# Performance work log

Hardware: AMD Instinct MI355X
Metric: run time of the kernel (lower is better)

The kernel has to match this reference:

```python
import jax, jax.numpy as jnp
import numpy as np

B, S, D, H, DH = 8192, 64, 32, 4, 8

def setup_inputs() -> dict:
    key = jax.random.key(0)
    ks = jax.random.split(key, 10)
    lim = 1.0 / np.sqrt(D)
    def lin(k):
        kw, kb = jax.random.split(k)
        W = jax.random.uniform(kw, (D, D), jnp.float32, -lim, lim)
        b = jax.random.uniform(kb, (D,), jnp.float32, -lim, lim)
        return W, b
    Wq, bq = lin(ks[0]); Wk, bk = lin(ks[1]); Wv, bv = lin(ks[2]); Wp, bp = lin(ks[3])
    x = jax.random.normal(ks[4], (B, S, D), jnp.float32)
    always_attend_upto = jax.random.randint(ks[5], (B,), 0, 64, jnp.int64 if jax.config.jax_enable_x64 else jnp.int32)
    return {"x": x, "always_attend_upto": always_attend_upto,
            "Wq": Wq, "bq": bq, "Wk": Wk, "bk": bk, "Wv": Wv, "bv": bv, "Wp": Wp, "bp": bp}

def reference(x, always_attend_upto, Wq, bq, Wk, bk, Wv, bv, Wp, bp):
    # QKV projections (torch Linear: y = x @ W.T + b)
    def heads(W, b):
        y = x @ W.T + b                      # [B,S,D]
        return y.reshape(B, S, H, DH).transpose(0, 2, 1, 3)  # [B,H,S,DH]
    q, k, v = heads(Wq, bq), heads(Wk, bk), heads(Wv, bv)
    score = jnp.einsum('bhqd,bhkd->bhqk', q, k) / jnp.sqrt(jnp.float32(DH))
    # prefix-LM mask: allowed if causal (j<=i) OR key in prefix (j < length[b])
    i = jnp.arange(S)[:, None]
    j = jnp.arange(S)[None, :]
    causal = j <= i                                        # [S,S]
    prefix = j[None, :, :] < always_attend_upto[:, None, None]  # [B,S,S]
    allowed = (causal[None] | prefix)[:, None, :, :]       # [B,1,S,S]
    score = jnp.where(allowed, score, -jnp.inf)
    attn = jax.nn.softmax(score, axis=-1)
    out = jnp.einsum('bhqk,bhkd->bhqd', attn, v)           # [B,H,S,DH]
    out = out.transpose(0, 2, 1, 3).reshape(B, S, D)
    return out @ Wp.T + bp
```

## Files before the change

### kernel.cpp

```cpp
#include <hip/hip_runtime.h>
#include <cstdint>
#include <cstddef>

#define NB 8192

typedef __attribute__((ext_vector_type(8))) short short8;
typedef __attribute__((ext_vector_type(4))) float f32x4;

union S8U { short8 s; unsigned u[4]; uint4 v; };
union FI { float f; int i; unsigned u; };

static __device__ __forceinline__ unsigned pk2(float a, float b) {
    unsigned short ua = __builtin_bit_cast(unsigned short, (__bf16)a);
    unsigned short ub = __builtin_bit_cast(unsigned short, (__bf16)b);
    return (unsigned)ua | ((unsigned)ub << 16);
}

#define MFMA __builtin_amdgcn_mfma_f32_16x16x32_bf16
#define BPERM __builtin_amdgcn_ds_bpermute
#define LDSFENCE() asm volatile("" ::: "memory")

__global__ __launch_bounds__(128, 4) void fused_attn_mfma(
    const float* __restrict__ x,
    const int*   __restrict__ aatt,
    const float* __restrict__ Wq, const float* __restrict__ bq,
    const float* __restrict__ Wk, const float* __restrict__ bk,
    const float* __restrict__ Wv, const float* __restrict__ bv,
    const float* __restrict__ Wp, const float* __restrict__ bp,
    float* __restrict__ out)
{
    __shared__ __align__(16) short klds[64][40];
    __shared__ __align__(16) short vbt[33][72];
    __shared__ __align__(16) short psl[2][16][40];

    const int tid  = threadIdx.x;
    const int w    = tid >> 6;
    const int lane = tid & 63;
    const int q4   = lane >> 4;
    const int l15  = lane & 15;
    const int b    = blockIdx.x;

    const int aab = aatt[b];
    const unsigned bmask = (q4 == 0) ? 0xFFFFFFFFu : 0u;

    int cmpv[4];
#pragma unroll
    for (int it = 0; it < 4; ++it) cmpv[it] = max(l15 + 16*it, aab - 1) - q4*4;

    short8 xa[4];
    const float* xb = x + (size_t)b * 64 * 32;
#pragma unroll
    for (int nt = 0; nt < 4; ++nt) {
        const float* p = xb + (nt*16 + l15)*32 + q4*8;
        float4 u0 = *(const float4*)p;
        float4 u1 = *(const float4*)(p + 4);
        S8U t;
        t.u[0] = pk2(u0.x, u0.y); t.u[1] = pk2(u0.z, u0.w);
        t.u[2] = pk2(u1.x, u1.y); t.u[3] = pk2(u1.z, u1.w);
        xa[nt] = t.s;
    }

    auto wrow = [&](const float* W, int row) -> short8 {
        const float* p = W + row*32 + q4*8;
        float4 u0 = *(const float4*)p;
        float4 u1 = *(const float4*)(p + 4);
        S8U t;
        t.u[0] = pk2(u0.x, u0.y); t.u[1] = pk2(u0.z, u0.w);
        t.u[2] = pk2(u1.x, u1.y); t.u[3] = pk2(u1.z, u1.w);
        return t.s;
    };

    const float escale = 0.35355339059327373f * 1.4426950408889634f;

    unsigned qpk01[4], qpk23[4];
    {
        short8 wa = wrow(Wq, 16*w + l15);
        float4 b4 = *(const float4*)(bq + 16*w + q4*4);
#pragma unroll
        for (int nt = 0; nt < 4; ++nt) {
            f32x4 acc = {0.f,0.f,0.f,0.f};
            acc = MFMA(wa, xa[nt], acc, 0,0,0);
            qpk01[nt] = pk2((acc[0]+b4.x)*escale, (acc[1]+b4.y)*escale);
            qpk23[nt] = pk2((acc[2]+b4.z)*escale, (acc[3]+b4.w)*escale);
        }
    }
    {
        short8 wa = wrow(Wk, 16*w + l15);
        float4 b4 = *(const float4*)(bk + 16*w + q4*4);
#pragma unroll
        for (int nt = 0; nt < 4; ++nt) {
            f32x4 acc = {0.f,0.f,0.f,0.f};
            acc = MFMA(wa, xa[nt], acc, 0,0,0);
            uint2 w2;
            w2.x = pk2(acc[0]+b4.x, acc[1]+b4.y);
            w2.y = pk2(acc[2]+b4.z, acc[3]+b4.w);
            *(uint2*)&klds[nt*16 + l15][16*w + q4*4] = w2;
        }
    }
    {
        short8 wv = wrow(Wv, 16*w + l15);
        const float bvv = bv[16*w + l15];
#pragma unroll
        for (int mt = 0; mt < 4; ++mt) {
            f32x4 acc = {0.f,0.f,0.f,0.f};
            acc = MFMA(xa[mt], wv, acc, 0,0,0);
            uint2 w2;
            w2.x = pk2(acc[0]+bvv, acc[1]+bvv);
            w2.y = pk2(acc[2]+bvv, acc[3]+bvv);
            *(uint2*)&vbt[16*w + l15][mt*16 + q4*4] = w2;
        }
    }
    if (q4 == 0) {
        uint2 ones; ones.x = 0x3F803F80u; ones.y = 0x3F803F80u;
        *(uint2*)&vbt[32][l15*4] = ones;
    }
    LDSFENCE();

    unsigned opk01s[2][4], opk23s[2][4];

#pragma unroll
    for (int hl = 0; hl < 2; ++hl) {
        const int idxA = (32*hl + l15) * 4;
        const int idxB = idxA + 64;

        short8 sqb[4];
#pragma unroll
        for (int it = 0; it < 4; ++it) {
            S8U t;
            t.u[0] = (unsigned)BPERM(idxA, (int)qpk01[it]) & bmask;
            t.u[1] = (unsigned)BPERM(idxA, (int)qpk23[it]) & bmask;
            t.u[2] = (unsigned)BPERM(idxB, (int)qpk01[it]) & bmask;
            t.u[3] = (unsigned)BPERM(idxB, (int)qpk23[it]) & bmask;
            sqb[it] = t.s;
        }

        const int avrow = (l15 < 8) ? (16*w + 8*hl + l15) : 32;
        const short* avbase = &vbt[avrow][0];

        f32x4 oacch[4];
#pragma unroll
        for (int it = 0; it < 4; ++it) oacch[it] = (f32x4){0.f,0.f,0.f,0.f};

#pragma unroll
        for (int jb = 0; jb < 2; ++jb) {
            short8 ska[2];
#pragma unroll
            for (int jt = 0; jt < 2; ++jt) {
                S8U t; t.v = *(const uint4*)&klds[jb*32 + jt*16 + l15][16*w + 8*hl];
                ska[jt] = t.s;
            }
            S8U av; av.v = *(const uint4*)&avbase[jb*32 + q4*8];

#pragma unroll
            for (int it = 0; it < 4; ++it) {
#pragma unroll
                for (int jt = 0; jt < 2; ++jt) {
                    f32x4 sacc = {0.f,0.f,0.f,0.f};
                    sacc = MFMA(ska[jt], sqb[it], sacc, 0,0,0);
                    float e[4];
#pragma unroll
                    for (int r = 0; r < 4; ++r) {
                        float ee = __builtin_amdgcn_exp2f(sacc[r]);
                        e[r] = (jb*32 + jt*16 + r <= cmpv[it]) ? ee : 0.0f;
                    }
                    uint2 pw; pw.x = pk2(e[0], e[1]); pw.y = pk2(e[2], e[3]);
                    *(uint2*)&psl[w][l15][jt*16 + q4*4] = pw;
                }
                LDSFENCE();
                S8U pb; pb.v = *(const uint4*)&psl[w][l15][q4*8];
                oacch[it] = MFMA(av.s, pb.s, oacch[it], 0,0,0);
                LDSFENCE();
            }
        }

#pragma unroll
        for (int it = 0; it < 4; ++it) {
            FI s; s.i = BPERM((32 + l15) * 4, __builtin_bit_cast(int, oacch[it][0]));
            const float inv = __builtin_amdgcn_rcpf(s.f);
            opk01s[hl][it] = pk2(oacch[it][0]*inv, oacch[it][1]*inv);
            opk23s[hl][it] = pk2(oacch[it][2]*inv, oacch[it][3]*inv);
        }
    }

    __syncthreads();
    if (q4 < 2) {
#pragma unroll
        for (int hl = 0; hl < 2; ++hl)
#pragma unroll
            for (int it = 0; it < 4; ++it) {
                uint2 ow; ow.x = opk01s[hl][it]; ow.y = opk23s[hl][it];
                *(uint2*)&klds[it*16 + l15][(2*w + hl)*8 + q4*4] = ow;
            }
    }
    __syncthreads();

    short8 wpb[2];
#pragma unroll
    for (int nt = 0; nt < 2; ++nt) wpb[nt] = wrow(Wp, nt*16 + l15);

    const float bpv[2] = { bp[l15], bp[16 + l15] };
    float* ob = out + (size_t)b * 64 * 32;
#pragma unroll
    for (int u = 0; u < 2; ++u) {
        S8U oa; oa.v = *(const uint4*)&klds[(2*w + u)*16 + l15][q4*8];
#pragma unroll
        for (int nt = 0; nt < 2; ++nt) {
            f32x4 y = {0.f,0.f,0.f,0.f};
            y = MFMA(oa.s, wpb[nt], y, 0,0,0);
#pragma unroll
            for (int r = 0; r < 4; ++r)
                ob[((2*w + u)*16 + q4*4 + r)*32 + nt*16 + l15] = y[r] + bpv[nt];
        }
    }
}

extern "C" void kernel_launch(void* const* d_in, const int* in_sizes, int n_in,
                              void* d_out, int out_size, void* d_ws, size_t ws_size,
                              hipStream_t stream) {
    const float* x  = (const float*)d_in[0];
    const int*   aa = (const int*)d_in[1];
    const float* Wq = (const float*)d_in[2];
    const float* bq = (const float*)d_in[3];
    const float* Wk = (const float*)d_in[4];
    const float* bk = (const float*)d_in[5];
    const float* Wv = (const float*)d_in[6];
    const float* bv = (const float*)d_in[7];
    const float* Wp = (const float*)d_in[8];
    const float* bp = (const float*)d_in[9];
    float* out = (float*)d_out;

    dim3 grid(NB), block(128);
    hipLaunchKernelGGL(fused_attn_mfma, grid, block, 0, stream,
                       x, aa, Wq, bq, Wk, bk, Wv, bv, Wp, bp, out);
}
```

Before: 50.69 us.

## Software-pipeline score and PV MFMAs with double-buffered probability LDS tiles

The attention inner loop is flattened into eight steps. The exp'd score tile is written into one of two LDS buffers while the PV MFMA consumes the previous step's tile, so the score MFMA, exp work and PV MFMA can overlap instead of serialising on one buffer. The compiler memory fences are removed and the V operands are loaded up front. Normalised outputs are now written straight into the K LDS region per head, which drops the register stash and the extra barrier, relying on each wave touching only its own columns. The cost is a doubled probability buffer and more live registers.

```diff
diff --git a/kernel.cpp b/kernel.cpp
--- a/kernel.cpp
+++ b/kernel.cpp
@@ -18,7 +18,6 @@
 
 #define MFMA __builtin_amdgcn_mfma_f32_16x16x32_bf16
 #define BPERM __builtin_amdgcn_ds_bpermute
-#define LDSFENCE() asm volatile("" ::: "memory")
 
 __global__ __launch_bounds__(128, 4) void fused_attn_mfma(
     const float* __restrict__ x,
@@ -31,7 +30,7 @@
 {
     __shared__ __align__(16) short klds[64][40];
     __shared__ __align__(16) short vbt[33][72];
-    __shared__ __align__(16) short psl[2][16][40];
+    __shared__ __align__(16) short psl[2][2][16][40];
 
     const int tid  = threadIdx.x;
     const int w    = tid >> 6;
@@ -114,9 +113,6 @@
         uint2 ones; ones.x = 0x3F803F80u; ones.y = 0x3F803F80u;
         *(uint2*)&vbt[32][l15*4] = ones;
     }
-    LDSFENCE();
-
-    unsigned opk01s[2][4], opk23s[2][4];
 
 #pragma unroll
     for (int hl = 0; hl < 2; ++hl) {
@@ -135,63 +131,55 @@
         }
 
         const int avrow = (l15 < 8) ? (16*w + 8*hl + l15) : 32;
-        const short* avbase = &vbt[avrow][0];
+        S8U av[2];
+        av[0].v = *(const uint4*)&vbt[avrow][q4*8];
+        av[1].v = *(const uint4*)&vbt[avrow][32 + q4*8];
 
         f32x4 oacch[4];
 #pragma unroll
         for (int it = 0; it < 4; ++it) oacch[it] = (f32x4){0.f,0.f,0.f,0.f};
 
 #pragma unroll
-        for (int jb = 0; jb < 2; ++jb) {
-            short8 ska[2];
+        for (int tk = 0; tk < 8; ++tk) {
+            const int jb = tk >> 2, it = tk & 3;
 #pragma unroll
             for (int jt = 0; jt < 2; ++jt) {
-                S8U t; t.v = *(const uint4*)&klds[jb*32 + jt*16 + l15][16*w + 8*hl];
-                ska[jt] = t.s;
+                S8U kt; kt.v = *(const uint4*)&klds[jb*32 + jt*16 + l15][16*w + 8*hl];
+                f32x4 sacc = {0.f,0.f,0.f,0.f};
+                sacc = MFMA(kt.s, sqb[it], sacc, 0,0,0);
+                float e[4];
+#pragma unroll
+                for (int r = 0; r < 4; ++r) {
+                    float ee = __builtin_amdgcn_exp2f(sacc[r]);
+                    e[r] = (jb*32 + jt*16 + r <= cmpv[it]) ? ee : 0.0f;
+                }
+                uint2 pw; pw.x = pk2(e[0], e[1]); pw.y = pk2(e[2], e[3]);
+                *(uint2*)&psl[w][tk & 1][l15][jt*16 + q4*4] = pw;
             }
-            S8U av; av.v = *(const uint4*)&avbase[jb*32 + q4*8];
-
-#pragma unroll
-            for (int it = 0; it < 4; ++it) {
-#pragma unroll
-                for (int jt = 0; jt < 2; ++jt) {
-                    f32x4 sacc = {0.f,0.f,0.f,0.f};
-                    sacc = MFMA(ska[jt], sqb[it], sacc, 0,0,0);
-                    float e[4];
-#pragma unroll
-                    for (int r = 0; r < 4; ++r) {
-                        float ee = __builtin_amdgcn_exp2f(sacc[r]);
-                        e[r] = (jb*32 + jt*16 + r <= cmpv[it]) ? ee : 0.0f;
-                    }
-                    uint2 pw; pw.x = pk2(e[0], e[1]); pw.y = pk2(e[2], e[3]);
-                    *(uint2*)&psl[w][l15][jt*16 + q4*4] = pw;
-                }
-                LDSFENCE();
-                S8U pb; pb.v = *(const uint4*)&psl[w][l15][q4*8];
-                oacch[it] = MFMA(av.s, pb.s, oacch[it], 0,0,0);
-                LDSFENCE();
+            if (tk > 0) {
+                const int pj = (tk - 1) >> 2, pi = (tk - 1) & 3;
+                S8U pb; pb.v = *(const uint4*)&psl[w][(tk - 1) & 1][l15][q4*8];
+                oacch[pi] = MFMA(av[pj].s, pb.s, oacch[pi], 0,0,0);
             }
+        }
+        {
+            S8U pb; pb.v = *(const uint4*)&psl[w][1][l15][q4*8];
+            oacch[3] = MFMA(av[1].s, pb.s, oacch[3], 0,0,0);
         }
 
 #pragma unroll
         for (int it = 0; it < 4; ++it) {
             FI s; s.i = BPERM((32 + l15) * 4, __builtin_bit_cast(int, oacch[it][0]));
             const float inv = __builtin_amdgcn_rcpf(s.f);
-            opk01s[hl][it] = pk2(oacch[it][0]*inv, oacch[it][1]*inv);
-            opk23s[hl][it] = pk2(oacch[it][2]*inv, oacch[it][3]*inv);
-        }
-    }
-
-    __syncthreads();
-    if (q4 < 2) {
-#pragma unroll
-        for (int hl = 0; hl < 2; ++hl)
-#pragma unroll
-            for (int it = 0; it < 4; ++it) {
-                uint2 ow; ow.x = opk01s[hl][it]; ow.y = opk23s[hl][it];
+            const unsigned o01 = pk2(oacch[it][0]*inv, oacch[it][1]*inv);
+            const unsigned o23 = pk2(oacch[it][2]*inv, oacch[it][3]*inv);
+            if (q4 < 2) {
+                uint2 ow; ow.x = o01; ow.y = o23;
                 *(uint2*)&klds[it*16 + l15][(2*w + hl)*8 + q4*4] = ow;
             }
-    }
+        }
+    }
+
     __syncthreads();
 
     short8 wpb[2];
```

Result: no change. 51.06 us (+0.7%).
